# Performance work log

Measured on AMD Instinct MI355X. Metric: run time of the kernel, lower is better.

The kernel has to match this reference:

```python
import jax, jax.numpy as jnp
import numpy as np

N_EMBEDDINGS = 1024
EMBEDDING_DIM = 256
DECAY = 0.99
EPSILON = 1e-05


def setup_inputs() -> dict:
    key = jax.random.key(0)
    k1, k2, k3 = jax.random.split(key, 3)
    inputs = jax.random.normal(k1, (16, 64, 64, EMBEDDING_DIM), dtype=jnp.float32)
    codebook = jax.random.normal(k2, (N_EMBEDDINGS, EMBEDDING_DIM), dtype=jnp.float32)
    ema_w = jax.random.normal(k3, (N_EMBEDDINGS, EMBEDDING_DIM), dtype=jnp.float32)
    ema_cluster_size = jnp.zeros((N_EMBEDDINGS,), dtype=jnp.float32)
    return {"inputs": inputs, "codebook": codebook, "ema_w": ema_w,
            "ema_cluster_size": ema_cluster_size}


def reference(inputs, codebook, ema_w, ema_cluster_size):
    input_shape = inputs.shape
    flat = inputs.reshape(-1, EMBEDDING_DIM)  # [N, D]
    # Squared Euclidean pairwise distances: [N, K]
    dists = (jnp.sum(flat * flat, axis=1, keepdims=True)
             + jnp.sum(codebook * codebook, axis=1)[None, :]
             - 2.0 * flat @ codebook.T)
    idx = jnp.argmin(dists, axis=1)  # [N]
    encodings = jax.nn.one_hot(idx, N_EMBEDDINGS, dtype=flat.dtype)  # [N, K]
    quantized = (encodings @ codebook).reshape(input_shape)
    # EMA updates (training mode)
    cs = ema_cluster_size * DECAY + (1.0 - DECAY) * jnp.sum(encodings, axis=0)
    n = jnp.sum(cs)
    cs = (cs + EPSILON) / (n + cs * EPSILON) * n  # faithful to original expression
    dw = encodings.T @ flat  # [K, D] scatter-accumulate via matmul
    new_ema_w = ema_w * DECAY + (1.0 - DECAY) * dw
    new_codebook = new_ema_w / cs[:, None]
    return quantized, encodings, cs, new_ema_w, new_codebook
```

## Files before the change

kernel.cpp:

```cpp
#include <hip/hip_runtime.h>

#define N_ROWS 65536
#define D 256
#define K 1024
#define DECAYF 0.99f
#define OMDF 0.01f
#define EPSF 1e-5f
#define MARGIN 0.5f

typedef _Float16 f16;
typedef _Float16 f16x8 __attribute__((ext_vector_type(8)));
typedef float f32x16 __attribute__((ext_vector_type(16)));
typedef float f32x4 __attribute__((ext_vector_type(4)));

__global__ __launch_bounds__(256) void prep_kernel(const float* __restrict__ cb,
                                                   float* __restrict__ cnorm,
                                                   char* __restrict__ wsB,
                                                   float* __restrict__ dw,
                                                   float* __restrict__ counts) {
    const int tid = threadIdx.x;
    const int bid = blockIdx.x;
    const int g = bid * 256 + tid;
    *reinterpret_cast<float4*>(dw + (size_t)g * 4) = make_float4(0.f, 0.f, 0.f, 0.f);
    if (g < K) counts[g] = 0.f;
    {
        const int row = bid * 4 + (tid >> 6);
        const int lane = tid & 63;
        const float4 v = *reinterpret_cast<const float4*>(cb + (size_t)row * D + lane * 4);
        float s = v.x * v.x + v.y * v.y + v.z * v.z + v.w * v.w;
        #pragma unroll
        for (int m = 32; m; m >>= 1) s += __shfl_xor(s, m);
        if (lane == 0) cnorm[row] = s;
    }
    if (g < 32768) {
        const int l31 = g & 31;
        const int h   = (g >> 5) & 1;
        const int cfg = (g >> 6) & 7;
        const int ks  = (g >> 9) & 3;
        const int dk  = (g >> 11) & 3;
        const int ct  = (g >> 13) & 3;
        const int code = ct * 256 + cfg * 32 + l31;
        const int dim0 = dk * 64 + ks * 16 + h * 8;
        const float* src = cb + (size_t)code * D + dim0;
        f16 out[8];
        #pragma unroll
        for (int e = 0; e < 8; ++e) out[e] = (f16)src[e];
        *reinterpret_cast<f16x8*>(wsB + (size_t)g * 16) = *reinterpret_cast<f16x8*>(out);
    }
}

__global__ __launch_bounds__(256, 3) void argmin_coarse_kernel(
        const float* __restrict__ x, const float* __restrict__ cb,
        const char* __restrict__ wsB, const float* __restrict__ cnorm,
        int* __restrict__ idx_out, float* __restrict__ counts) {
    __shared__ char smem[43264];
    char* Alds = smem;
    char* Blds = smem + 8192;
    unsigned short* cand = reinterpret_cast<unsigned short*>(smem + 40960);
    int* ccnt = reinterpret_cast<int*>(smem + 43008);
    const int tid = threadIdx.x;
    const int wave = tid >> 6;
    const int lane = tid & 63;
    const int l31 = lane & 31;
    const int h = lane >> 5;
    const int rw = wave >> 1;
    const int cw = wave & 1;
    const int n0 = blockIdx.x * 64;

    if (tid < 64) ccnt[tid] = 0;

    const int s_row = tid >> 2;
    const int c4 = tid & 3;
    const int ssw = s_row & 7;
    char* s_rowbase = Alds + s_row * 128;

    const int arow = rw * 32 + l31;
    const int asw = arow & 7;
    char* abase = Alds + arow * 128;

    float B_run[16];
    #pragma unroll
    for (int r = 0; r < 16; ++r) B_run[r] = 3.4e38f;

    #pragma unroll 1
    for (int ct = 0; ct < 4; ++ct) {
        f32x16 acc[4];
        #pragma unroll
        for (int cf = 0; cf < 4; ++cf)
            #pragma unroll
            for (int r = 0; r < 16; ++r) acc[cf][r] = 0.f;

        #pragma unroll 1
        for (int dks = 0; dks < 4; ++dks) {
            const int dk = (ct & 1) ? (3 - dks) : dks;
            __syncthreads();
            if (!(ct > 0 && dks == 0)) {
                const float4 f0 = *reinterpret_cast<const float4*>(
                    x + (size_t)(n0 + s_row) * D + dk * 64 + c4 * 16);
                const float4 f1 = *reinterpret_cast<const float4*>(
                    x + (size_t)(n0 + s_row) * D + dk * 64 + c4 * 16 + 4);
                const float4 f2 = *reinterpret_cast<const float4*>(
                    x + (size_t)(n0 + s_row) * D + dk * 64 + c4 * 16 + 8);
                const float4 f3 = *reinterpret_cast<const float4*>(
                    x + (size_t)(n0 + s_row) * D + dk * 64 + c4 * 16 + 12);
                f16 hi8a[8] = {(f16)f0.x, (f16)f0.y, (f16)f0.z, (f16)f0.w,
                               (f16)f1.x, (f16)f1.y, (f16)f1.z, (f16)f1.w};
                f16 hi8b[8] = {(f16)f2.x, (f16)f2.y, (f16)f2.z, (f16)f2.w,
                               (f16)f3.x, (f16)f3.y, (f16)f3.z, (f16)f3.w};
                *reinterpret_cast<f16x8*>(s_rowbase + (((c4 * 2 + 0) ^ ssw) * 16)) = *reinterpret_cast<f16x8*>(hi8a);
                *reinterpret_cast<f16x8*>(s_rowbase + (((c4 * 2 + 1) ^ ssw) * 16)) = *reinterpret_cast<f16x8*>(hi8b);
            }
            {
                const int4* gsrc = reinterpret_cast<const int4*>(wsB + (size_t)(ct * 4 + dk) * 32768);
                int4* ldst = reinterpret_cast<int4*>(Blds);
                #pragma unroll
                for (int i = 0; i < 8; ++i) ldst[tid + i * 256] = gsrc[tid + i * 256];
            }
            __syncthreads();
            #pragma unroll
            for (int ks = 0; ks < 4; ++ks) {
                const int sA = ks * 2 + h;
                const f16x8 Ah = *reinterpret_cast<const f16x8*>(abase + ((sA ^ asw) * 16));
                #pragma unroll
                for (int cf = 0; cf < 4; ++cf) {
                    const f16x8 Bh = *reinterpret_cast<const f16x8*>(
                        Blds + (size_t)(ks * 8 + cw * 4 + cf) * 1024 + lane * 16);
                    acc[cf] = __builtin_amdgcn_mfma_f32_32x32x16_f16(Ah, Bh, acc[cf], 0, 0, 0);
                }
            }
        }
        const int codebase = ct * 256 + cw * 128;
        float cn[4];
        #pragma unroll
        for (int cf = 0; cf < 4; ++cf) cn[cf] = cnorm[codebase + cf * 32 + l31];
        #pragma unroll
        for (int r = 0; r < 16; ++r) {
            float d[4];
            float m = 3.4e38f;
            #pragma unroll
            for (int cf = 0; cf < 4; ++cf) {
                d[cf] = cn[cf] - 2.f * acc[cf][r];
                m = fminf(m, d[cf]);
            }
            #pragma unroll
            for (int msk = 16; msk; msk >>= 1) m = fminf(m, __shfl_xor(m, msk));
            const float br = fminf(B_run[r], m);
            B_run[r] = br;
            const float lim = br + MARGIN;
            const int row = rw * 32 + (r & 3) + 8 * (r >> 2) + 4 * h;
            #pragma unroll
            for (int cf = 0; cf < 4; ++cf) {
                if (d[cf] <= lim) {
                    const int pos = atomicAdd(&ccnt[row], 1);
                    if (pos < 16) cand[row * 16 + pos] = (unsigned short)(codebase + cf * 32 + l31);
                }
            }
        }
    }
    __syncthreads();
    #pragma unroll 1
    for (int rr = 0; rr < 16; ++rr) {
        const int row = wave * 16 + rr;
        const int n = ccnt[row];
        const f32x4 xv = *reinterpret_cast<const f32x4*>(x + (size_t)(n0 + row) * D + lane * 4);
        float bd = 3.4e38f;
        int bi = K;
        if (n <= 16) {
            for (int j = 0; j < n; ++j) {
                const int code = cand[row * 16 + j];
                const f32x4 cv = *reinterpret_cast<const f32x4*>(cb + (size_t)code * D + lane * 4);
                float s = xv[0] * cv[0] + xv[1] * cv[1] + xv[2] * cv[2] + xv[3] * cv[3];
                #pragma unroll
                for (int msk = 32; msk; msk >>= 1) s += __shfl_xor(s, msk);
                const float dd = cnorm[code] - 2.f * s;
                if (dd < bd || (dd == bd && code < bi)) { bd = dd; bi = code; }
            }
        } else {
            for (int code = 0; code < K; ++code) {
                const f32x4 cv = *reinterpret_cast<const f32x4*>(cb + (size_t)code * D + lane * 4);
                float s = xv[0] * cv[0] + xv[1] * cv[1] + xv[2] * cv[2] + xv[3] * cv[3];
                #pragma unroll
                for (int msk = 32; msk; msk >>= 1) s += __shfl_xor(s, msk);
                const float dd = cnorm[code] - 2.f * s;
                if (dd < bd) { bd = dd; bi = code; }
            }
        }
        if (lane == 0) {
            idx_out[n0 + row] = bi;
            atomicAdd(&counts[bi], 1.0f);
        }
    }
}

__global__ __launch_bounds__(256) void quant_kernel(const float* __restrict__ cb,
                                                    const int* __restrict__ idx,
                                                    float* __restrict__ quant) {
    const int n = blockIdx.x * 4 + (threadIdx.x >> 6);
    const int lane = threadIdx.x & 63;
    const int i = idx[n];
    const f32x4 c = *reinterpret_cast<const f32x4*>(cb + (size_t)i * D + lane * 4);
    __builtin_nontemporal_store(c, reinterpret_cast<f32x4*>(quant + (size_t)n * D + lane * 4));
}

__global__ __launch_bounds__(256) void enc_kernel(const int* __restrict__ idx,
                                                  float* __restrict__ enc) {
    const int total = N_ROWS * (K / 4);
    for (int g = blockIdx.x * blockDim.x + threadIdx.x; g < total;
         g += gridDim.x * blockDim.x) {
        const int n = g >> 8;
        const int k0 = (g & 255) * 4;
        const int i = idx[n];
        f32x4 v;
        v[0] = (k0 == i) ? 1.f : 0.f;
        v[1] = (k0 + 1 == i) ? 1.f : 0.f;
        v[2] = (k0 + 2 == i) ? 1.f : 0.f;
        v[3] = (k0 + 3 == i) ? 1.f : 0.f;
        __builtin_nontemporal_store(v, reinterpret_cast<f32x4*>(enc + (size_t)g * 4));
    }
}

__global__ __launch_bounds__(1024) void cs_scan_kernel(const float* __restrict__ ema_cs,
                                                       const float* __restrict__ counts,
                                                       float* __restrict__ cs_out,
                                                       int* __restrict__ cursor) {
    __shared__ float wsum[16];
    __shared__ int wisum[16];
    __shared__ float n_sh;
    const int k = threadIdx.x;
    const int wid = k >> 6;
    const int lane = k & 63;
    const float cnt = counts[k];
    const float c = ema_cs[k] * DECAYF + OMDF * cnt;
    const int ic = (int)cnt;
    int v = ic;
    #pragma unroll
    for (int d = 1; d < 64; d <<= 1) {
        const int t = __shfl_up(v, d);
        if (lane >= d) v += t;
    }
    float s = c;
    #pragma unroll
    for (int m = 32; m; m >>= 1) s += __shfl_xor(s, m);
    if (lane == 63) wisum[wid] = v;
    if (lane == 0) wsum[wid] = s;
    __syncthreads();
    if (k == 0) {
        float n = 0.f;
        for (int w = 0; w < 16; ++w) n += wsum[w];
        n_sh = n;
    }
    if (wid == 0 && lane < 16) {
        int wv = wisum[lane];
        #pragma unroll
        for (int d = 1; d < 16; d <<= 1) {
            const int t = __shfl_up(wv, d);
            if (lane >= d) wv += t;
        }
        wisum[lane] = wv;
    }
    __syncthreads();
    const float n = n_sh;
    cs_out[k] = (c + EPSF) / (n + c * EPSF) * n;
    const int wbase = (wid == 0) ? 0 : wisum[wid - 1];
    cursor[k] = wbase + v - ic;
}

__global__ __launch_bounds__(256) void scatter_kernel(const int* __restrict__ idx,
                                                      int* __restrict__ cursor,
                                                      int* __restrict__ rowlist,
                                                      int* __restrict__ codelist) {
    __shared__ int hist[1024];
    const int tid = threadIdx.x;
    #pragma unroll
    for (int j = 0; j < 4; ++j) hist[tid + j * 256] = 0;
    __syncthreads();
    const int n = blockIdx.x * 256 + tid;
    const int i = idx[n];
    atomicAdd(&hist[i], 1);
    __syncthreads();
    #pragma unroll
    for (int j = 0; j < 4; ++j) {
        const int k = tid + j * 256;
        const int c = hist[k];
        hist[k] = (c > 0) ? atomicAdd(&cursor[k], c) : 0;
    }
    __syncthreads();
    const int pos = atomicAdd(&hist[i], 1);
    rowlist[pos] = n;
    codelist[pos] = i;
}

__global__ __launch_bounds__(256) void chunk_sum_kernel(const float* __restrict__ x,
                                                        const int* __restrict__ rowlist,
                                                        const int* __restrict__ codelist,
                                                        float* __restrict__ dw) {
    const int wave = threadIdx.x >> 6;
    const int lane = threadIdx.x & 63;
    const int p0 = blockIdx.x * 32 + wave * 8;
    int rows[8], codes[8];
    #pragma unroll
    for (int j = 0; j < 8; ++j) {
        rows[j] = rowlist[p0 + j];
        codes[j] = codelist[p0 + j];
    }
    f32x4 v[8];
    #pragma unroll
    for (int j = 0; j < 8; ++j)
        v[j] = __builtin_nontemporal_load(
            reinterpret_cast<const f32x4*>(x + (size_t)rows[j] * D + lane * 4));
    f32x4 s = v[0];
    int cur = codes[0];
    #pragma unroll
    for (int j = 1; j < 8; ++j) {
        if (codes[j] != cur) {
            float* dst = dw + (size_t)cur * D + lane * 4;
            atomicAdd(dst + 0, s[0]); atomicAdd(dst + 1, s[1]);
            atomicAdd(dst + 2, s[2]); atomicAdd(dst + 3, s[3]);
            cur = codes[j];
            s = v[j];
        } else {
            s[0] += v[j][0]; s[1] += v[j][1]; s[2] += v[j][2]; s[3] += v[j][3];
        }
    }
    float* dst = dw + (size_t)cur * D + lane * 4;
    atomicAdd(dst + 0, s[0]); atomicAdd(dst + 1, s[1]);
    atomicAdd(dst + 2, s[2]); atomicAdd(dst + 3, s[3]);
}

__global__ __launch_bounds__(256) void ema_kernel(const float* __restrict__ ema_w,
                                                  const float* __restrict__ dw,
                                                  const float* __restrict__ cs,
                                                  float* __restrict__ w_out,
                                                  float* __restrict__ cb_out) {
    const int e4 = blockIdx.x * blockDim.x + threadIdx.x;
    const int k = e4 >> 6;
    const float csk = cs[k];
    const float4 w = *reinterpret_cast<const float4*>(ema_w + (size_t)e4 * 4);
    const float4 d = *reinterpret_cast<const float4*>(dw + (size_t)e4 * 4);
    float4 nw, nc;
    nw.x = w.x * DECAYF + OMDF * d.x;
    nw.y = w.y * DECAYF + OMDF * d.y;
    nw.z = w.z * DECAYF + OMDF * d.z;
    nw.w = w.w * DECAYF + OMDF * d.w;
    nc.x = nw.x / csk; nc.y = nw.y / csk; nc.z = nw.z / csk; nc.w = nw.w / csk;
    *reinterpret_cast<float4*>(w_out + (size_t)e4 * 4) = nw;
    *reinterpret_cast<float4*>(cb_out + (size_t)e4 * 4) = nc;
}

extern "C" void kernel_launch(void* const* d_in, const int* in_sizes, int n_in,
                              void* d_out, int out_size, void* d_ws, size_t ws_size,
                              hipStream_t stream) {
    (void)in_sizes; (void)n_in; (void)out_size; (void)ws_size;
    const float* x      = (const float*)d_in[0];
    const float* cb     = (const float*)d_in[1];
    const float* ema_w  = (const float*)d_in[2];
    const float* ema_cs = (const float*)d_in[3];

    float* out    = (float*)d_out;
    float* quant  = out;
    float* enc    = quant + 16777216;
    float* cs_out = enc + 67108864;
    float* w_out  = cs_out + 1024;
    float* cb_out = w_out + 262144;

    float* ws       = (float*)d_ws;
    float* counts   = ws;
    float* dw       = ws + 1024;
    float* cnorm    = ws + 263168;
    int*   cursor   = (int*)(ws + 264192);
    int*   idx      = (int*)(ws + 265216);
    int*   rowlist  = (int*)(ws + 330752);
    int*   codelist = (int*)(ws + 396288);
    char*  wsB      = (char*)(ws + 461824);

    prep_kernel<<<256, 256, 0, stream>>>(cb, cnorm, wsB, dw, counts);
    argmin_coarse_kernel<<<N_ROWS / 64, 256, 0, stream>>>(x, cb, wsB, cnorm, idx, counts);
    quant_kernel<<<N_ROWS / 4, 256, 0, stream>>>(cb, idx, quant);
    enc_kernel<<<2048, 256, 0, stream>>>(idx, enc);
    cs_scan_kernel<<<1, 1024, 0, stream>>>(ema_cs, counts, cs_out, cursor);
    scatter_kernel<<<N_ROWS / 256, 256, 0, stream>>>(idx, cursor, rowlist, codelist);
    chunk_sum_kernel<<<2048, 256, 0, stream>>>(x, rowlist, codelist, dw);
    ema_kernel<<<65536 / 256, 256, 0, stream>>>(ema_w, dw, cs_out, w_out, cb_out);
}
```

Before: 357.3 us.

## Double-buffer codebook tiles with register prefetch and keep full A row in LDS

Result: slower. 388.5 us (+8.7%).

```diff
diff --git a/kernel.cpp b/kernel.cpp
--- a/kernel.cpp
+++ b/kernel.cpp
@@ -34,13 +34,12 @@
     }
     if (g < 32768) {
         const int l31 = g & 31;
-        const int h   = (g >> 5) & 1;
-        const int cfg = (g >> 6) & 7;
-        const int ks  = (g >> 9) & 3;
-        const int dk  = (g >> 11) & 3;
-        const int ct  = (g >> 13) & 3;
-        const int code = ct * 256 + cfg * 32 + l31;
-        const int dim0 = dk * 64 + ks * 16 + h * 8;
+        const int cfg = (g >> 5) & 3;
+        const int sA  = (g >> 7) & 7;
+        const int dk  = (g >> 10) & 3;
+        const int cg  = g >> 12;
+        const int code = cg * 128 + cfg * 32 + l31;
+        const int dim0 = dk * 64 + sA * 8;
         const float* src = cb + (size_t)code * D + dim0;
         f16 out[8];
         #pragma unroll
@@ -49,15 +48,16 @@
     }
 }
 
-__global__ __launch_bounds__(256, 3) void argmin_coarse_kernel(
+__global__ __launch_bounds__(256, 2) void argmin_coarse_kernel(
         const float* __restrict__ x, const float* __restrict__ cb,
         const char* __restrict__ wsB, const float* __restrict__ cnorm,
         int* __restrict__ idx_out, float* __restrict__ counts) {
-    __shared__ char smem[43264];
+    __shared__ char smem[67840];
     char* Alds = smem;
-    char* Blds = smem + 8192;
-    unsigned short* cand = reinterpret_cast<unsigned short*>(smem + 40960);
-    int* ccnt = reinterpret_cast<int*>(smem + 43008);
+    char* Bbuf0 = smem + 32768;
+    char* Bbuf1 = smem + 49152;
+    unsigned short* cand = reinterpret_cast<unsigned short*>(smem + 65536);
+    int* ccnt = reinterpret_cast<int*>(smem + 67584);
     const int tid = threadIdx.x;
     const int wave = tid >> 6;
     const int lane = tid & 63;
@@ -69,95 +69,107 @@
 
     if (tid < 64) ccnt[tid] = 0;
 
-    const int s_row = tid >> 2;
-    const int c4 = tid & 3;
-    const int ssw = s_row & 7;
-    char* s_rowbase = Alds + s_row * 128;
+    {
+        const int s_row = tid >> 2;
+        const int c4 = tid & 3;
+        const float* src = x + (size_t)(n0 + s_row) * D + c4 * 64;
+        char* rowbase = Alds + s_row * 512;
+        const int sw = s_row & 7;
+        #pragma unroll
+        for (int j = 0; j < 8; ++j) {
+            const float4 fa = *reinterpret_cast<const float4*>(src + j * 8);
+            const float4 fb = *reinterpret_cast<const float4*>(src + j * 8 + 4);
+            f16 h8[8] = {(f16)fa.x, (f16)fa.y, (f16)fa.z, (f16)fa.w,
+                         (f16)fb.x, (f16)fb.y, (f16)fb.z, (f16)fb.w};
+            const int ph = c4 * 8 + (j ^ sw);
+            *reinterpret_cast<f16x8*>(rowbase + ph * 16) = *reinterpret_cast<f16x8*>(h8);
+        }
+        const int4* gsrc = reinterpret_cast<const int4*>(wsB);
+        int4* ldst = reinterpret_cast<int4*>(Bbuf0);
+        #pragma unroll
+        for (int i = 0; i < 4; ++i) ldst[tid + i * 256] = gsrc[tid + i * 256];
+    }
+    __syncthreads();
 
     const int arow = rw * 32 + l31;
+    char* abase = Alds + arow * 512;
     const int asw = arow & 7;
-    char* abase = Alds + arow * 128;
 
     float B_run[16];
     #pragma unroll
     for (int r = 0; r < 16; ++r) B_run[r] = 3.4e38f;
 
+    int cur = 0;
     #pragma unroll 1
-    for (int ct = 0; ct < 4; ++ct) {
-        f32x16 acc[4];
-        #pragma unroll
-        for (int cf = 0; cf < 4; ++cf)
+    for (int cg = 0; cg < 8; ++cg) {
+        f32x16 acc[2];
+        #pragma unroll
+        for (int cf = 0; cf < 2; ++cf)
             #pragma unroll
             for (int r = 0; r < 16; ++r) acc[cf][r] = 0.f;
 
         #pragma unroll 1
-        for (int dks = 0; dks < 4; ++dks) {
-            const int dk = (ct & 1) ? (3 - dks) : dks;
+        for (int dk = 0; dk < 4; ++dk) {
+            const int p = cg * 4 + dk;
+            int4 pre0, pre1, pre2, pre3;
+            if (p < 31) {
+                const int4* gsrc = reinterpret_cast<const int4*>(wsB + (size_t)(p + 1) * 16384);
+                pre0 = gsrc[tid];
+                pre1 = gsrc[tid + 256];
+                pre2 = gsrc[tid + 512];
+                pre3 = gsrc[tid + 768];
+            }
+            {
+                const char* Bcur = cur ? Bbuf1 : Bbuf0;
+                #pragma unroll
+                for (int ks = 0; ks < 4; ++ks) {
+                    const int sA = ks * 2 + h;
+                    const f16x8 Ah = *reinterpret_cast<const f16x8*>(
+                        abase + (dk * 8 + (sA ^ asw)) * 16);
+                    #pragma unroll
+                    for (int cf = 0; cf < 2; ++cf) {
+                        const f16x8 Bh = *reinterpret_cast<const f16x8*>(
+                            Bcur + ((sA * 4 + cw * 2 + cf) * 32 + l31) * 16);
+                        acc[cf] = __builtin_amdgcn_mfma_f32_32x32x16_f16(Ah, Bh, acc[cf], 0, 0, 0);
+                    }
+                }
+            }
+            if (p < 31) {
+                int4* ldst = reinterpret_cast<int4*>(cur ? Bbuf0 : Bbuf1);
+                ldst[tid] = pre0;
+                ldst[tid + 256] = pre1;
+                ldst[tid + 512] = pre2;
+                ldst[tid + 768] = pre3;
+            }
+            if (dk == 3) {
+                const int codebase = cg * 128 + cw * 64;
+                const float cn0 = cnorm[codebase + l31];
+                const float cn1 = cnorm[codebase + 32 + l31];
+                #pragma unroll
+                for (int r = 0; r < 16; ++r) {
+                    const float d0 = cn0 - 2.f * acc[0][r];
+                    const float d1 = cn1 - 2.f * acc[1][r];
+                    float m = fminf(d0, d1);
+                    #pragma unroll
+                    for (int msk = 16; msk; msk >>= 1) m = fminf(m, __shfl_xor(m, msk));
+                    const float br = fminf(B_run[r], m);
+                    B_run[r] = br;
+                    const float lim = br + MARGIN;
+                    const int row = rw * 32 + (r & 3) + 8 * (r >> 2) + 4 * h;
+                    if (d0 <= lim) {
+                        const int pos = atomicAdd(&ccnt[row], 1);
+                        if (pos < 16) cand[row * 16 + pos] = (unsigned short)(codebase + l31);
+                    }
+                    if (d1 <= lim) {
+                        const int pos = atomicAdd(&ccnt[row], 1);
+                        if (pos < 16) cand[row * 16 + pos] = (unsigned short)(codebase + 32 + l31);
+                    }
+                }
+            }
             __syncthreads();
-            if (!(ct > 0 && dks == 0)) {
-                const float4 f0 = *reinterpret_cast<const float4*>(
-                    x + (size_t)(n0 + s_row) * D + dk * 64 + c4 * 16);
-                const float4 f1 = *reinterpret_cast<const float4*>(
-                    x + (size_t)(n0 + s_row) * D + dk * 64 + c4 * 16 + 4);
-                const float4 f2 = *reinterpret_cast<const float4*>(
-                    x + (size_t)(n0 + s_row) * D + dk * 64 + c4 * 16 + 8);
-                const float4 f3 = *reinterpret_cast<const float4*>(
-                    x + (size_t)(n0 + s_row) * D + dk * 64 + c4 * 16 + 12);
-                f16 hi8a[8] = {(f16)f0.x, (f16)f0.y, (f16)f0.z, (f16)f0.w,
-                               (f16)f1.x, (f16)f1.y, (f16)f1.z, (f16)f1.w};
-                f16 hi8b[8] = {(f16)f2.x, (f16)f2.y, (f16)f2.z, (f16)f2.w,
-                               (f16)f3.x, (f16)f3.y, (f16)f3.z, (f16)f3.w};
-                *reinterpret_cast<f16x8*>(s_rowbase + (((c4 * 2 + 0) ^ ssw) * 16)) = *reinterpret_cast<f16x8*>(hi8a);
-                *reinterpret_cast<f16x8*>(s_rowbase + (((c4 * 2 + 1) ^ ssw) * 16)) = *reinterpret_cast<f16x8*>(hi8b);
-            }
-            {
-                const int4* gsrc = reinterpret_cast<const int4*>(wsB + (size_t)(ct * 4 + dk) * 32768);
-                int4* ldst = reinterpret_cast<int4*>(Blds);
-                #pragma unroll
-                for (int i = 0; i < 8; ++i) ldst[tid + i * 256] = gsrc[tid + i * 256];
-            }
-            __syncthreads();
-            #pragma unroll
-            for (int ks = 0; ks < 4; ++ks) {
-                const int sA = ks * 2 + h;
-                const f16x8 Ah = *reinterpret_cast<const f16x8*>(abase + ((sA ^ asw) * 16));
-                #pragma unroll
-                for (int cf = 0; cf < 4; ++cf) {
-                    const f16x8 Bh = *reinterpret_cast<const f16x8*>(
-                        Blds + (size_t)(ks * 8 + cw * 4 + cf) * 1024 + lane * 16);
-                    acc[cf] = __builtin_amdgcn_mfma_f32_32x32x16_f16(Ah, Bh, acc[cf], 0, 0, 0);
-                }
-            }
-        }
-        const int codebase = ct * 256 + cw * 128;
-        float cn[4];
-        #pragma unroll
-        for (int cf = 0; cf < 4; ++cf) cn[cf] = cnorm[codebase + cf * 32 + l31];
-        #pragma unroll
-        for (int r = 0; r < 16; ++r) {
-            float d[4];
-            float m = 3.4e38f;
-            #pragma unroll
-            for (int cf = 0; cf < 4; ++cf) {
-                d[cf] = cn[cf] - 2.f * acc[cf][r];
-                m = fminf(m, d[cf]);
-            }
-            #pragma unroll
-            for (int msk = 16; msk; msk >>= 1) m = fminf(m, __shfl_xor(m, msk));
-            const float br = fminf(B_run[r], m);
-            B_run[r] = br;
-            const float lim = br + MARGIN;
-            const int row = rw * 32 + (r & 3) + 8 * (r >> 2) + 4 * h;
-            #pragma unroll
-            for (int cf = 0; cf < 4; ++cf) {
-                if (d[cf] <= lim) {
-                    const int pos = atomicAdd(&ccnt[row], 1);
-                    if (pos < 16) cand[row * 16 + pos] = (unsigned short)(codebase + cf * 32 + l31);
-                }
-            }
-        }
-    }
-    __syncthreads();
+            cur ^= 1;
+        }
+    }
     #pragma unroll 1
     for (int rr = 0; rr < 16; ++rr) {
         const int row = wave * 16 + rr;
```
